# Optimization experiments

Hardware: AMD Instinct MI355X
Metric: run time of the kernel (lower is better)

## Reference

```python
import jax, jax.numpy as jnp
import numpy as np

ALPHA = 2.0  # ATan surrogate alpha (spikingjelly default)
V_TH = 1.0   # v_threshold
H = 8        # num_heads

@jax.custom_vjp
def atan_spike(x):
    # heaviside(v - v_th); x = v - v_th
    return (x >= 0.0).astype(x.dtype)

def _spike_fwd(x):
    return atan_spike(x), x

def _spike_bwd(x, g):
    pi_half = jnp.asarray(np.pi / 2, x.dtype)
    grad = (ALPHA / 2.0) / (1.0 + (pi_half * ALPHA * x) ** 2)
    return (g * grad,)

atan_spike.defvjp(_spike_fwd, _spike_bwd)

def lif(x_seq, w):
    # MultiStepParametricLIFNode: recurrence over leading dim of x_seq.
    # v <- v + (x - (v - v_reset)) * sigmoid(w); v_reset = 0; hard reset, detach_reset=True.
    sg = jax.nn.sigmoid(w)
    def step(v, x):
        h = v + (x - v) * sg
        s = atan_spike(h - V_TH)
        v_new = h * (1.0 - jax.lax.stop_gradient(s))  # hard reset to 0, detached spike
        return v_new, s
    v0 = jnp.zeros_like(x_seq[0])
    _, spikes = jax.lax.scan(step, v0, x_seq)
    return spikes


def setup_inputs() -> dict:
    key = jax.random.key(0)
    ks = jax.random.split(key, 6)
    T, B, N, C = 4, 32, 196, 512
    s = 0.02
    return {
        "x": jax.random.normal(ks[0], (T, B, N, C), dtype=jnp.float32),
        "Wq": jax.random.normal(ks[1], (C, C), dtype=jnp.float32) * s,
        "Wk": jax.random.normal(ks[2], (C, C), dtype=jnp.float32) * s,
        "Wv": jax.random.normal(ks[3], (C, C), dtype=jnp.float32) * s,
        "Wp": jax.random.normal(ks[4], (C, C), dtype=jnp.float32) * s,
        "bp": jax.random.normal(ks[5], (C,), dtype=jnp.float32) * s,
        "wq": jnp.zeros((), jnp.float32),  # init_tau=2 -> w=0
        "wk": jnp.zeros((), jnp.float32),
        "wv": jnp.zeros((), jnp.float32),
        "wa": jnp.zeros((), jnp.float32),
        "wp": jnp.zeros((), jnp.float32),
    }


def reference(x, Wq, Wk, Wv, Wp, bp, wq, wk, wv, wa, wp):
    T, B, N, C = x.shape
    d = C // H
    scale = d ** (-0.5)
    xf = x.reshape(T * B, N, C)  # LIF steps over T*B (faithful to original flatten(0,1))

    def qkv(W, w_lif):
        y = lif(xf @ W.T, w_lif)                       # [T*B, N, C] binary spikes
        return y.reshape(T, B, N, H, d).transpose(0, 1, 3, 2, 4)  # [T,B,H,N,d]

    q = qkv(Wq, wq)
    k = qkv(Wk, wk)
    v = qkv(Wv, wv)

    attn = jnp.einsum('tbhnd,tbhmd->tbhnm', q, k) * scale   # softmax-free
    y = jnp.einsum('tbhnm,tbhmd->tbhnd', attn, v)           # [T,B,H,N,d]
    y = y.swapaxes(3, 4).reshape(T, B, N, C)                # faithful transpose(3,4).reshape

    y = lif(y, wa)                                          # attn_lif steps over T
    out = lif(y.reshape(T * B, N, C) @ Wp.T + bp, wp)       # proj_lif steps over T*B
    return out.reshape(T, B, N, C)
```

## Files before the change

kernel.cpp:

```cpp
#include <hip/hip_runtime.h>
#include <hip/hip_bf16.h>

#define NC 100352
typedef unsigned long long ull;
typedef float (*tile_t)[132];

template <bool PROJ>
__global__ __launch_bounds__(256) void gemm_lif(
    const float* __restrict__ A,
    const float* __restrict__ W0, const float* __restrict__ W1,
    const float* __restrict__ W2, const float* __restrict__ bias,
    const float* __restrict__ w0, const float* __restrict__ w1,
    const float* __restrict__ w2,
    ull* __restrict__ M, float* __restrict__ out)
{
    __shared__ float U[128][132];
    tile_t As0 = (tile_t)&U[0][0];
    tile_t As1 = (tile_t)&U[16][0];
    tile_t Bs0 = (tile_t)&U[32][0];
    tile_t Bs1 = (tile_t)&U[48][0];

    const int bid = blockIdx.x;
    int n, cb, br;
    if (PROJ) {
        const int work = (bid & 7) * 98 + (bid >> 3);
        n = work >> 2; cb = work & 3; br = 0;
    } else {
        const int work = (bid & 7) * 294 + (bid >> 3);
        n = work / 12; const int r12 = work - n * 12;
        br = r12 >> 2; cb = r12 & 3;
    }
    const float* Wb   = PROJ ? W0 : (br == 0 ? W0 : (br == 1 ? W1 : W2));
    const float* wsel = PROJ ? w0 : (br == 0 ? w0 : (br == 1 ? w1 : w2));

    const int tid = threadIdx.x;
    const int r0 = tid >> 2;
    const int kq = (tid & 3) << 2;
    const int rg = (tid >> 4) << 2;
    const int cg = (tid & 15) << 2;

    const float* Ap0 = A + (size_t)r0 * NC + n * 512 + kq;
    const float* Ap1 = Ap0 + (size_t)64 * NC;
    const float* Wq0 = Wb + (size_t)(cb * 128 + r0) * 512 + kq;
    const float* Wq1 = Wq0 + (size_t)64 * 512;

    float acc[8][8] = {};
    float4 sa0, sa1, sb0, sb1;

    auto LOAD = [&](int k) {
        sa0 = *(const float4*)(Ap0 + k);
        sa1 = *(const float4*)(Ap1 + k);
        sb0 = *(const float4*)(Wq0 + k);
        sb1 = *(const float4*)(Wq1 + k);
    };
    auto STORE = [&](tile_t A_, tile_t B_) {
        A_[kq + 0][r0] = sa0.x; A_[kq + 1][r0] = sa0.y;
        A_[kq + 2][r0] = sa0.z; A_[kq + 3][r0] = sa0.w;
        A_[kq + 0][r0 + 64] = sa1.x; A_[kq + 1][r0 + 64] = sa1.y;
        A_[kq + 2][r0 + 64] = sa1.z; A_[kq + 3][r0 + 64] = sa1.w;
        B_[kq + 0][r0] = sb0.x; B_[kq + 1][r0] = sb0.y;
        B_[kq + 2][r0] = sb0.z; B_[kq + 3][r0] = sb0.w;
        B_[kq + 0][r0 + 64] = sb1.x; B_[kq + 1][r0 + 64] = sb1.y;
        B_[kq + 2][r0 + 64] = sb1.z; B_[kq + 3][r0 + 64] = sb1.w;
    };
    auto COMP = [&](const tile_t A_, const tile_t B_) {
#pragma unroll
        for (int k = 0; k < 16; ++k) {
            float av[8], bv[8];
            *(float4*)&av[0] = *(const float4*)&A_[k][rg];
            *(float4*)&av[4] = *(const float4*)&A_[k][rg + 64];
            *(float4*)&bv[0] = *(const float4*)&B_[k][cg];
            *(float4*)&bv[4] = *(const float4*)&B_[k][cg + 64];
#pragma unroll
            for (int i = 0; i < 8; ++i)
#pragma unroll
                for (int j = 0; j < 8; ++j)
                    acc[i][j] = fmaf(av[i], bv[j], acc[i][j]);
        }
    };

    LOAD(0); STORE(As0, Bs0);
    __syncthreads();
    for (int kk = 0; kk < 512; kk += 32) {
        LOAD(kk + 16);
        COMP(As0, Bs0);
        STORE(As1, Bs1);
        __syncthreads();
        if (kk + 32 < 512) {
            LOAD(kk + 32);
            COMP(As1, Bs1);
            STORE(As0, Bs0);
        } else {
            COMP(As1, Bs1);
        }
        __syncthreads();
    }

#pragma unroll
    for (int ih = 0; ih < 2; ++ih)
#pragma unroll
        for (int i = 0; i < 4; ++i) {
            const int row = rg + i + ih * 64;
#pragma unroll
            for (int jh = 0; jh < 2; ++jh) {
                float4 o;
                o.x = acc[ih * 4 + i][jh * 4 + 0];
                o.y = acc[ih * 4 + i][jh * 4 + 1];
                o.z = acc[ih * 4 + i][jh * 4 + 2];
                o.w = acc[ih * 4 + i][jh * 4 + 3];
                if (PROJ) {
                    const int colb = cb * 128 + cg + jh * 64;
                    o.x += bias[colb + 0]; o.y += bias[colb + 1];
                    o.z += bias[colb + 2]; o.w += bias[colb + 3];
                }
                *(float4*)&U[row][cg + jh * 64] = o;
            }
        }
    __syncthreads();

    if (tid < 128) {
        const float sg = 1.0f / (1.0f + expf(-wsel[0]));
        const int c = tid, lane = tid & 63;
        const int hglob = cb * 2 + (c >> 6);
        ull* Mw = M + (size_t)br * 200704 + (size_t)hglob * 196 + n;
        float* Ow = out + (size_t)n * 512 + cb * 128 + c;
        float v = 0.0f;
        for (int tb = 0; tb < 128; ++tb) {
            const float uu = U[tb][c];
            const float hh = __fadd_rn(v, __fmul_rn(__fsub_rn(uu, v), sg));
            const bool sp = hh >= 1.0f;
            if (PROJ) {
                Ow[(size_t)tb * NC] = sp ? 1.0f : 0.0f;
            } else {
                const ull mm = __ballot(sp);
                if (lane == 0) Mw[(size_t)tb * 1568] = mm;
            }
            v = sp ? 0.0f : hh;
        }
    }
}

__global__ __launch_bounds__(256) void attn_fused(const ull* __restrict__ Qm,
                                                  const ull* __restrict__ Km,
                                                  const ull* __restrict__ Vm,
                                                  const float* __restrict__ wa,
                                                  float* __restrict__ Y)
{
    const int b = blockIdx.x >> 3;
    const int h = blockIdx.x & 7;
    const int tid = threadIdx.x;
    const int w = tid >> 6;
    const int lane = tid & 63;

    __shared__ ull qrow[256], krow[256], vrow[256];
    __shared__ ull kcol[64][5], vcol[64][5];
    __shared__ ushort G[64][64];
    __shared__ float vstate[196][64];
    __shared__ ull sbm[208];

    const float sg = 1.0f / (1.0f + expf(-wa[0]));

    for (int t = 0; t < 4; ++t) {
        const int tb = t * 32 + b;
        const size_t mb = (size_t)tb * 1568 + (size_t)h * 196;
        if (tid < 196) {
            qrow[tid] = Qm[mb + tid];
            krow[tid] = Km[mb + tid];
            vrow[tid] = Vm[mb + tid];
        } else {
            qrow[tid] = 0; krow[tid] = 0; vrow[tid] = 0;
        }
        __syncthreads();

        {
            ull kc = 0, vc = 0;
#pragma unroll 8
            for (int m = 0; m < 64; ++m) {
                kc |= ((krow[w * 64 + m] >> lane) & 1ull) << m;
                vc |= ((vrow[w * 64 + m] >> lane) & 1ull) << m;
            }
            kcol[lane][w] = kc; vcol[lane][w] = vc;
        }
        __syncthreads();

        for (int p = tid; p < 4096; p += 256) {
            const int d1 = p >> 6, d2 = p & 63;
            const int g = __popcll(kcol[d1][0] & vcol[d2][0]) +
                          __popcll(kcol[d1][1] & vcol[d2][1]) +
                          __popcll(kcol[d1][2] & vcol[d2][2]) +
                          __popcll(kcol[d1][3] & vcol[d2][3]);
            G[d1][d2] = (ushort)g;
        }
        __syncthreads();

        {
            int r = 49 * w;
            const int rend = r + 49;
            for (; r + 1 < rend; r += 2) {
                const ull q0 = qrow[r], q1 = qrow[r + 1];
                const uint a0 = (uint)q0, a1 = (uint)(q0 >> 32);
                const uint b0 = (uint)q1, b1 = (uint)(q1 >> 32);
                uint s0 = 0, s1 = 0;
#pragma unroll
                for (int d = 0; d < 32; ++d) {
                    const uint g = G[d][lane];
                    s0 += ((a0 >> d) & 1u) * g;
                    s1 += ((b0 >> d) & 1u) * g;
                }
#pragma unroll
                for (int d = 0; d < 32; ++d) {
                    const uint g = G[32 + d][lane];
                    s0 += ((a1 >> d) & 1u) * g;
                    s1 += ((b1 >> d) & 1u) * g;
                }
                const float y0 = (float)s0 * 0.125f;
                const float v0 = t ? vstate[r][lane] : 0.0f;
                const float h0 = __fadd_rn(v0, __fmul_rn(__fsub_rn(y0, v0), sg));
                const bool sp0 = h0 >= 1.0f;
                vstate[r][lane] = sp0 ? 0.0f : h0;
                const ull m0 = __ballot(sp0);
                const float y1 = (float)s1 * 0.125f;
                const float v1 = t ? vstate[r + 1][lane] : 0.0f;
                const float h1 = __fadd_rn(v1, __fmul_rn(__fsub_rn(y1, v1), sg));
                const bool sp1 = h1 >= 1.0f;
                vstate[r + 1][lane] = sp1 ? 0.0f : h1;
                const ull m1 = __ballot(sp1);
                if (lane == 0) { sbm[r] = m0; sbm[r + 1] = m1; }
            }
            {
                const ull q0 = qrow[r];
                const uint a0 = (uint)q0, a1 = (uint)(q0 >> 32);
                uint s0 = 0;
#pragma unroll
                for (int d = 0; d < 32; ++d) s0 += ((a0 >> d) & 1u) * (uint)G[d][lane];
#pragma unroll
                for (int d = 0; d < 32; ++d) s0 += ((a1 >> d) & 1u) * (uint)G[32 + d][lane];
                const float y0 = (float)s0 * 0.125f;
                const float v0 = t ? vstate[r][lane] : 0.0f;
                const float h0 = __fadd_rn(v0, __fmul_rn(__fsub_rn(y0, v0), sg));
                const bool sp0 = h0 >= 1.0f;
                vstate[r][lane] = sp0 ? 0.0f : h0;
                const ull m0 = __ballot(sp0);
                if (lane == 0) sbm[r] = m0;
            }
        }
        __syncthreads();

        const size_t yb = (size_t)tb * NC + (size_t)h * 12544;
        for (int f = tid; f < 12544; f += 256) {
            const int e = f / 196;
            const int r2 = f - e * 196;
            Y[yb + f] = ((sbm[r2] >> e) & 1ull) ? 1.0f : 0.0f;
        }
        __syncthreads();
    }
}

extern "C" void kernel_launch(void* const* d_in, const int* in_sizes, int n_in,
                              void* d_out, int out_size, void* d_ws, size_t ws_size,
                              hipStream_t stream) {
    const float* x  = (const float*)d_in[0];
    const float* Wq = (const float*)d_in[1];
    const float* Wk = (const float*)d_in[2];
    const float* Wv = (const float*)d_in[3];
    const float* Wp = (const float*)d_in[4];
    const float* bp = (const float*)d_in[5];
    const float* wq = (const float*)d_in[6];
    const float* wk = (const float*)d_in[7];
    const float* wv = (const float*)d_in[8];
    const float* wa = (const float*)d_in[9];
    const float* wp = (const float*)d_in[10];
    float* out = (float*)d_out;

    char* ws = (char*)d_ws;
    ull* Qm = (ull*)ws;
    ull* Km = Qm + 200704;
    ull* Vm = Km + 200704;
    float* ySc = (float*)(ws + (size_t)3 * 1605632);

    gemm_lif<false><<<2352, 256, 0, stream>>>(x, Wq, Wk, Wv, nullptr,
                                              wq, wk, wv, Qm, nullptr);

    attn_fused<<<256, 256, 0, stream>>>(Qm, Km, Vm, wa, ySc);

    gemm_lif<true><<<784, 256, 0, stream>>>(ySc, Wp, nullptr, nullptr, bp,
                                            wp, nullptr, nullptr, nullptr, out);
}
```

Baseline: 955.1 us.

## Unfuse LIF from GEMM and use larger 256x128 GEMM tiles

The fused GEMM+LIF kernel is split into a plain NT GEMM with 256x128 output tiles (16x8 accumulators per thread, launch bounds 2) and separate LIF kernels that scan the 128 T*B steps with fully parallel threads. Previously only 128 of 256 threads ran the serial LIF scan while the tile sat in shared memory. The change also enlarges the per-block tile to raise arithmetic intensity. In exchange it writes and rereads large fp32 intermediates (three 51 MB buffers plus the projection output) through global memory.

```diff
diff --git a/kernel.cpp b/kernel.cpp
--- a/kernel.cpp
+++ b/kernel.cpp
@@ -1,142 +1,157 @@
 #include <hip/hip_runtime.h>
-#include <hip/hip_bf16.h>
 
 #define NC 100352
 typedef unsigned long long ull;
-typedef float (*tile_t)[132];
-
-template <bool PROJ>
-__global__ __launch_bounds__(256) void gemm_lif(
+
+template <int NMAT, bool BIAS>
+__global__ __launch_bounds__(256, 2) void gemm_nt_big(
     const float* __restrict__ A,
     const float* __restrict__ W0, const float* __restrict__ W1,
     const float* __restrict__ W2, const float* __restrict__ bias,
-    const float* __restrict__ w0, const float* __restrict__ w1,
-    const float* __restrict__ w2,
-    ull* __restrict__ M, float* __restrict__ out)
+    float* __restrict__ C0, float* __restrict__ C1, float* __restrict__ C2)
 {
-    __shared__ float U[128][132];
-    tile_t As0 = (tile_t)&U[0][0];
-    tile_t As1 = (tile_t)&U[16][0];
-    tile_t Bs0 = (tile_t)&U[32][0];
-    tile_t Bs1 = (tile_t)&U[48][0];
-
-    const int bid = blockIdx.x;
-    int n, cb, br;
-    if (PROJ) {
-        const int work = (bid & 7) * 98 + (bid >> 3);
-        n = work >> 2; cb = work & 3; br = 0;
-    } else {
-        const int work = (bid & 7) * 294 + (bid >> 3);
-        n = work / 12; const int r12 = work - n * 12;
-        br = r12 >> 2; cb = r12 & 3;
-    }
-    const float* Wb   = PROJ ? W0 : (br == 0 ? W0 : (br == 1 ? W1 : W2));
-    const float* wsel = PROJ ? w0 : (br == 0 ? w0 : (br == 1 ? w1 : w2));
+    __shared__ float As[2][16][260];
+    __shared__ float Bs[2][16][132];
+
+    const int chunk = (NMAT * 392) >> 3;
+    const int w = (blockIdx.x & 7) * chunk + (blockIdx.x >> 3);
+    const int mb = w / (4 * NMAT);
+    const int rem = w - mb * (4 * NMAT);
+    const int br = rem >> 2;
+    const int cb = rem & 3;
+
+    const float* Wb = (NMAT == 1 || br == 0) ? W0 : (br == 1 ? W1 : W2);
+    float* Cb = (NMAT == 1 || br == 0) ? C0 : (br == 1 ? C1 : C2);
 
     const int tid = threadIdx.x;
-    const int r0 = tid >> 2;
-    const int kq = (tid & 3) << 2;
-    const int rg = (tid >> 4) << 2;
-    const int cg = (tid & 15) << 2;
-
-    const float* Ap0 = A + (size_t)r0 * NC + n * 512 + kq;
-    const float* Ap1 = Ap0 + (size_t)64 * NC;
-    const float* Wq0 = Wb + (size_t)(cb * 128 + r0) * 512 + kq;
-    const float* Wq1 = Wq0 + (size_t)64 * 512;
-
-    float acc[8][8] = {};
-    float4 sa0, sa1, sb0, sb1;
-
-    auto LOAD = [&](int k) {
-        sa0 = *(const float4*)(Ap0 + k);
-        sa1 = *(const float4*)(Ap1 + k);
-        sb0 = *(const float4*)(Wq0 + k);
-        sb1 = *(const float4*)(Wq1 + k);
+    const int q   = (tid & 3) << 2;
+    const int sr  = tid >> 2;
+    const int rg4 = (tid >> 4) << 2;
+    const int cg4 = (tid & 15) << 2;
+
+    const float* Ap = A  + (size_t)(mb * 256 + sr) * 512 + q;
+    const float* Bp = Wb + (size_t)(cb * 128 + sr) * 512 + q;
+
+    float acc[16][8] = {};
+    float4 a4[4], b4[2];
+
+    auto LOAD = [&](int k0) {
+#pragma unroll
+        for (int s = 0; s < 4; ++s)
+            a4[s] = *(const float4*)(Ap + (size_t)s * 64 * 512 + k0);
+#pragma unroll
+        for (int s = 0; s < 2; ++s)
+            b4[s] = *(const float4*)(Bp + (size_t)s * 64 * 512 + k0);
     };
-    auto STORE = [&](tile_t A_, tile_t B_) {
-        A_[kq + 0][r0] = sa0.x; A_[kq + 1][r0] = sa0.y;
-        A_[kq + 2][r0] = sa0.z; A_[kq + 3][r0] = sa0.w;
-        A_[kq + 0][r0 + 64] = sa1.x; A_[kq + 1][r0 + 64] = sa1.y;
-        A_[kq + 2][r0 + 64] = sa1.z; A_[kq + 3][r0 + 64] = sa1.w;
-        B_[kq + 0][r0] = sb0.x; B_[kq + 1][r0] = sb0.y;
-        B_[kq + 2][r0] = sb0.z; B_[kq + 3][r0] = sb0.w;
-        B_[kq + 0][r0 + 64] = sb1.x; B_[kq + 1][r0 + 64] = sb1.y;
-        B_[kq + 2][r0 + 64] = sb1.z; B_[kq + 3][r0 + 64] = sb1.w;
+    auto STORE = [&](int buf) {
+#pragma unroll
+        for (int s = 0; s < 4; ++s) {
+            As[buf][q + 0][sr + s * 64] = a4[s].x;
+            As[buf][q + 1][sr + s * 64] = a4[s].y;
+            As[buf][q + 2][sr + s * 64] = a4[s].z;
+            As[buf][q + 3][sr + s * 64] = a4[s].w;
+        }
+#pragma unroll
+        for (int s = 0; s < 2; ++s) {
+            Bs[buf][q + 0][sr + s * 64] = b4[s].x;
+            Bs[buf][q + 1][sr + s * 64] = b4[s].y;
+            Bs[buf][q + 2][sr + s * 64] = b4[s].z;
+            Bs[buf][q + 3][sr + s * 64] = b4[s].w;
+        }
     };
-    auto COMP = [&](const tile_t A_, const tile_t B_) {
+    auto COMP = [&](int buf) {
 #pragma unroll
         for (int k = 0; k < 16; ++k) {
-            float av[8], bv[8];
-            *(float4*)&av[0] = *(const float4*)&A_[k][rg];
-            *(float4*)&av[4] = *(const float4*)&A_[k][rg + 64];
-            *(float4*)&bv[0] = *(const float4*)&B_[k][cg];
-            *(float4*)&bv[4] = *(const float4*)&B_[k][cg + 64];
-#pragma unroll
-            for (int i = 0; i < 8; ++i)
+            float av[16], bv[8];
+#pragma unroll
+            for (int s = 0; s < 4; ++s)
+                *(float4*)&av[s * 4] = *(const float4*)&As[buf][k][rg4 + s * 64];
+#pragma unroll
+            for (int s = 0; s < 2; ++s)
+                *(float4*)&bv[s * 4] = *(const float4*)&Bs[buf][k][cg4 + s * 64];
+#pragma unroll
+            for (int i = 0; i < 16; ++i)
 #pragma unroll
                 for (int j = 0; j < 8; ++j)
                     acc[i][j] = fmaf(av[i], bv[j], acc[i][j]);
         }
     };
 
-    LOAD(0); STORE(As0, Bs0);
+    LOAD(0);
+    STORE(0);
     __syncthreads();
-    for (int kk = 0; kk < 512; kk += 32) {
-        LOAD(kk + 16);
-        COMP(As0, Bs0);
-        STORE(As1, Bs1);
-        __syncthreads();
-        if (kk + 32 < 512) {
-            LOAD(kk + 32);
-            COMP(As1, Bs1);
-            STORE(As0, Bs0);
+    int cur = 0;
+    for (int k0 = 0; k0 < 512; k0 += 16) {
+        if (k0 + 16 < 512) {
+            LOAD(k0 + 16);
+            COMP(cur);
+            STORE(cur ^ 1);
         } else {
-            COMP(As1, Bs1);
-        }
-        __syncthreads();
+            COMP(cur);
+        }
+        __syncthreads();
+        cur ^= 1;
     }
 
 #pragma unroll
-    for (int ih = 0; ih < 2; ++ih)
+    for (int s = 0; s < 4; ++s)
 #pragma unroll
         for (int i = 0; i < 4; ++i) {
-            const int row = rg + i + ih * 64;
-#pragma unroll
-            for (int jh = 0; jh < 2; ++jh) {
+            const int row = mb * 256 + rg4 + i + s * 64;
+#pragma unroll
+            for (int half = 0; half < 2; ++half) {
+                const int col = cb * 128 + cg4 + half * 64;
                 float4 o;
-                o.x = acc[ih * 4 + i][jh * 4 + 0];
-                o.y = acc[ih * 4 + i][jh * 4 + 1];
-                o.z = acc[ih * 4 + i][jh * 4 + 2];
-                o.w = acc[ih * 4 + i][jh * 4 + 3];
-                if (PROJ) {
-                    const int colb = cb * 128 + cg + jh * 64;
-                    o.x += bias[colb + 0]; o.y += bias[colb + 1];
-                    o.z += bias[colb + 2]; o.w += bias[colb + 3];
+                o.x = acc[s * 4 + i][half * 4 + 0];
+                o.y = acc[s * 4 + i][half * 4 + 1];
+                o.z = acc[s * 4 + i][half * 4 + 2];
+                o.w = acc[s * 4 + i][half * 4 + 3];
+                if (BIAS) {
+                    o.x += bias[col + 0]; o.y += bias[col + 1];
+                    o.z += bias[col + 2]; o.w += bias[col + 3];
                 }
-                *(float4*)&U[row][cg + jh * 64] = o;
+                *(float4*)&Cb[(size_t)row * 512 + col] = o;
             }
         }
-    __syncthreads();
-
-    if (tid < 128) {
-        const float sg = 1.0f / (1.0f + expf(-wsel[0]));
-        const int c = tid, lane = tid & 63;
-        const int hglob = cb * 2 + (c >> 6);
-        ull* Mw = M + (size_t)br * 200704 + (size_t)hglob * 196 + n;
-        float* Ow = out + (size_t)n * 512 + cb * 128 + c;
-        float v = 0.0f;
-        for (int tb = 0; tb < 128; ++tb) {
-            const float uu = U[tb][c];
-            const float hh = __fadd_rn(v, __fmul_rn(__fsub_rn(uu, v), sg));
-            const bool sp = hh >= 1.0f;
-            if (PROJ) {
-                Ow[(size_t)tb * NC] = sp ? 1.0f : 0.0f;
-            } else {
-                const ull mm = __ballot(sp);
-                if (lane == 0) Mw[(size_t)tb * 1568] = mm;
-            }
-            v = sp ? 0.0f : hh;
-        }
+}
+
+__global__ __launch_bounds__(256) void lif_mask3(
+    const float* __restrict__ U0, const float* __restrict__ U1,
+    const float* __restrict__ U2,
+    const float* __restrict__ wq, const float* __restrict__ wk,
+    const float* __restrict__ wv, ull* __restrict__ M)
+{
+    const int br = blockIdx.x / 392;
+    const int blk = blockIdx.x - br * 392;
+    const int i = blk * 256 + threadIdx.x;
+    const float* U = (br == 0) ? U0 : (br == 1 ? U1 : U2);
+    const float wv_ = (br == 0) ? wq[0] : (br == 1 ? wk[0] : wv[0]);
+    const float sg = 1.0f / (1.0f + expf(-wv_));
+    ull* Mw = M + (size_t)br * 200704 + ((i >> 6) & 7) * 196 + (i >> 9);
+    float v = 0.0f;
+    for (int t = 0; t < 128; ++t) {
+        const float x = U[(size_t)t * NC + i];
+        const float h = __fadd_rn(v, __fmul_rn(__fsub_rn(x, v), sg));
+        const bool sp = (h >= 1.0f);
+        const ull m = __ballot(sp);
+        if ((threadIdx.x & 63) == 0) Mw[(size_t)t * 1568] = m;
+        v = sp ? 0.0f : h;
+    }
+}
+
+__global__ __launch_bounds__(256) void lif_out(const float* __restrict__ U,
+                                               const float* __restrict__ wp,
+                                               float* __restrict__ out)
+{
+    const int i = blockIdx.x * 256 + threadIdx.x;
+    const float sg = 1.0f / (1.0f + expf(-wp[0]));
+    float v = 0.0f;
+    for (int t = 0; t < 128; ++t) {
+        const float x = U[(size_t)t * NC + i];
+        const float h = __fadd_rn(v, __fmul_rn(__fsub_rn(x, v), sg));
+        const bool sp = (h >= 1.0f);
+        out[(size_t)t * NC + i] = sp ? 1.0f : 0.0f;
+        v = sp ? 0.0f : h;
     }
 }
 
@@ -273,16 +288,22 @@
     float* out = (float*)d_out;
 
     char* ws = (char*)d_ws;
-    ull* Qm = (ull*)ws;
-    ull* Km = Qm + 200704;
-    ull* Vm = Km + 200704;
-    float* ySc = (float*)(ws + (size_t)3 * 1605632);
-
-    gemm_lif<false><<<2352, 256, 0, stream>>>(x, Wq, Wk, Wv, nullptr,
-                                              wq, wk, wv, Qm, nullptr);
+    float* u0 = (float*)ws;
+    float* u1 = (float*)(ws + (size_t)51380224);
+    float* u2 = (float*)(ws + (size_t)2 * 51380224);
+    ull* Qm   = (ull*)(ws + (size_t)3 * 51380224);
+    ull* Km   = Qm + 200704;
+    ull* Vm   = Km + 200704;
+    float* ySc = u0;
+    float* up  = u1;
+
+    gemm_nt_big<3, false><<<1176, 256, 0, stream>>>(x, Wq, Wk, Wv, nullptr,
+                                                    u0, u1, u2);
+    lif_mask3<<<1176, 256, 0, stream>>>(u0, u1, u2, wq, wk, wv, Qm);
 
     attn_fused<<<256, 256, 0, stream>>>(Qm, Km, Vm, wa, ySc);
 
-    gemm_lif<true><<<784, 256, 0, stream>>>(ySc, Wp, nullptr, nullptr, bp,
-                                            wp, nullptr, nullptr, nullptr, out);
-}
+    gemm_nt_big<1, true><<<392, 256, 0, stream>>>(ySc, Wp, nullptr, nullptr, bp,
+                                                  up, nullptr, nullptr);
+    lif_out<<<392, 256, 0, stream>>>(up, wp, out);
+}
```

Result: slower. 1.747 ms (+82.9%).
